# Optimization experiments

Hardware: AMD Instinct MI355X
Metric: run time of the kernel (lower is better)

The kernel has to match this reference:

```python
import jax, jax.numpy as jnp
import numpy as np

ROPE_BASE = 10000.0
CHUNK = 2048
NEG_INF = -1e30


def _rope(q, k, start_index):
    # q, k: (B, T, H, Dh) with Dh even; half-split RoPE as in RotaryEmbedding
    B, T, H, Dh = q.shape
    half = Dh // 2
    inv_freq = jnp.exp(jnp.arange(half, dtype=jnp.float32) * (-(np.log(ROPE_BASE) / half)))
    pos = jnp.arange(T, dtype=jnp.float32) + jnp.float32(start_index)
    ang = pos[:, None] * inv_freq[None, :]              # (T, half)
    cos = jnp.cos(ang)[None, :, None, :].astype(q.dtype)  # (1,T,1,half)
    sin = jnp.sin(ang)[None, :, None, :].astype(q.dtype)

    def rot(x):
        x1, x2 = x[..., :half], x[..., half:]
        return jnp.concatenate([x1 * cos - x2 * sin, x2 * cos + x1 * sin], axis=-1)

    return rot(q), rot(k)


def reference(q, k, v, start_index):
    # Chunked causal self-attention, softmax(QK^T) V with scale = 1.0 (Megalodon Eq. 9).
    B, T, H, Dh = q.shape
    Dv = v.shape[-1]
    q, k = _rope(q, k, start_index)

    nc = T // CHUNK  # T assumed multiple of chunk_size (prefill path, no cache)
    qc = q.reshape(B, nc, CHUNK, H, Dh)
    kc = k.reshape(B, nc, CHUNK, H, Dh)
    vc = v.reshape(B, nc, CHUNK, H, Dv)

    # per-chunk causal mask (C, C): 0 where j <= i else -inf
    i = jnp.arange(CHUNK)
    causal = (i[None, :] <= i[:, None])

    scores = jnp.einsum('bnqhd,bnkhd->bnhqk', qc, kc)  # scale = 1.0
    scores = jnp.where(causal[None, None, None, :, :], scores, NEG_INF)
    probs = jax.nn.softmax(scores, axis=-1)
    out = jnp.einsum('bnhqk,bnkhd->bnqhd', probs, vc)
    return out.reshape(B, T, H, Dv)


def setup_inputs() -> dict:
    key = jax.random.key(0)
    kq, kk, kv = jax.random.split(key, 3)
    B, T, H, Dh, Dv = 2, 4096, 16, 128, 128
    return {
        'q': jax.random.normal(kq, (B, T, H, Dh), dtype=jnp.float32),
        'k': jax.random.normal(kk, (B, T, H, Dh), dtype=jnp.float32),
        'v': jax.random.normal(kv, (B, T, H, Dv), dtype=jnp.float32),
        'start_index': 0,
    }
```

## Files before the change

### kernel.cpp

```cpp
#include <hip/hip_runtime.h>


#define T_TOT  4096
#define HH     16
#define DH     128
#define CHUNKL 2048
#define QT     128
#define KTILE  64
#define NEGV   1e30f
#define L2E    1.44269504088896f
#define THRL2  11.5415603f

typedef _Float16 f16;
typedef __attribute__((ext_vector_type(8)))  _Float16 f16x8;
typedef __attribute__((ext_vector_type(4)))  _Float16 f16x4;
typedef __attribute__((ext_vector_type(4)))  float    f32x4;

#define AS_G(p) ((const __attribute__((address_space(1))) void*)(p))
#define AS_L(p) ((__attribute__((address_space(3))) void*)(p))

__device__ __forceinline__ f32x4 mfma16(f16x8 a, f16x8 b, f32x4 c) {
    return __builtin_amdgcn_mfma_f32_16x16x32_f16(a, b, c, 0, 0, 0);
}

__global__ void rope_table_kernel(float* __restrict__ tab, const int* __restrict__ startp) {
    int gid = blockIdx.x * blockDim.x + threadIdx.x;
    int t = gid >> 6, d = gid & 63;
    float pos  = (float)(t + *startp);
    float invf = expf((float)d * (-9.210340371976184f / 64.0f));
    float s, c;
    sincosf(pos * invf, &s, &c);
    tab[gid] = c;
    tab[T_TOT * 64 + gid] = s;
}

__global__ void prep_kv_kernel(const float* __restrict__ K, const float* __restrict__ V,
                               const float* __restrict__ tab,
                               f16* __restrict__ Kws, f16* __restrict__ VTws) {
    const int half = (2 * T_TOT * HH * DH) / 8;
    int gid = blockIdx.x * blockDim.x + threadIdx.x;
    if (gid < half) {
        const int tile = gid >> 10, idx = gid & 1023;
        const int key = idx >> 4, c8 = idx & 15;
        const int dsw0 = c8 << 3;
        const int d0   = dsw0 ^ ((key & 15) << 3);
        const int kt = tile & 31, h = (tile >> 5) & 15, n = (tile >> 9) & 1, b = tile >> 10;
        const int t  = n * CHUNKL + kt * KTILE + key;
        const float* kp = K + ((size_t)(b * T_TOT + t) * HH + h) * DH;
        const int dl = d0 & 63;
        f32x4 xm0 = *(const f32x4*)(kp + d0);
        f32x4 xm1 = *(const f32x4*)(kp + d0 + 4);
        f32x4 xo0 = *(const f32x4*)(kp + (d0 ^ 64));
        f32x4 xo1 = *(const f32x4*)(kp + (d0 ^ 64) + 4);
        f32x4 cc0 = *(const f32x4*)(tab + t * 64 + dl);
        f32x4 cc1 = *(const f32x4*)(tab + t * 64 + dl + 4);
        f32x4 ss0 = *(const f32x4*)(tab + T_TOT * 64 + t * 64 + dl);
        f32x4 ss1 = *(const f32x4*)(tab + T_TOT * 64 + t * 64 + dl + 4);
        const float sgn = (d0 < 64) ? -1.f : 1.f;
        f16x8 out;
#pragma unroll
        for (int j = 0; j < 4; ++j) {
            out[j]     = (f16)(xm0[j] * cc0[j] + sgn * xo0[j] * ss0[j]);
            out[4 + j] = (f16)(xm1[j] * cc1[j] + sgn * xo1[j] * ss1[j]);
        }
        *(f16x8*)&Kws[(size_t)tile * 8192 + key * DH + dsw0] = out;
    } else {
        const int oc = gid - half;
        const int tile = oc >> 10, idx = oc & 1023;
        const int d = idx >> 3, c8 = idx & 7;
        const int ksw0 = c8 << 3;
        const int key0 = ksw0 ^ ((d & 7) << 3);
        const int kt = tile & 31, h = (tile >> 5) & 15, n = (tile >> 9) & 1, b = tile >> 10;
        const int t0 = n * CHUNKL + kt * KTILE + key0;
        const float* vp = V + ((size_t)(b * T_TOT + t0) * HH + h) * DH + d;
        f16x8 out;
#pragma unroll
        for (int j = 0; j < 8; ++j)
            out[j] = (f16)vp[(size_t)j * (HH * DH)];
        *(f16x8*)&VTws[(size_t)tile * 8192 + d * KTILE + ksw0] = out;
    }
}

__global__ __launch_bounds__(512, 4)
void attn_fast_kernel(const float* __restrict__ Q, const f16* __restrict__ Kws,
                      const f16* __restrict__ VTws, const float* __restrict__ tab,
                      float* __restrict__ O)
{
    __shared__ f16 Kl[2][KTILE * DH];
    __shared__ f16 VTl[2][KTILE * DH];
    __shared__ f16 Pl[8][16 * 64];

    const int bid = blockIdx.x;
    const int sb  = (bid & 7) * 128 + (bid >> 3);
    const int qt  = 15 - (sb & 15);
    const int bnh = sb >> 4;
    const int hd = bnh & 15, n = (bnh >> 4) & 1, b = bnh >> 5;

    const int tid = threadIdx.x;
    const int w   = tid >> 6;
    const int l   = tid & 63;
    const int g   = l >> 4;
    const int m   = l & 15;

    const int q0 = qt * QT;
    const size_t bh = (size_t)b * T_TOT * (HH * DH) + (size_t)hd * DH;
    const size_t tile0 = (size_t)bnh * (32 * 8192);

    const int qr = q0 + w * 16 + m;
    const int tg = n * CHUNKL + qr;
    const float* qp = Q + bh + (size_t)tg * (HH * DH);

    f16x8 qf[4];
#pragma unroll
    for (int kc = 0; kc < 4; ++kc) {
        const int dbase = kc * 32 + g * 8;
        const int dl    = dbase & 63;
        f32x4 xa0 = *(const f32x4*)(qp + dbase);
        f32x4 xa1 = *(const f32x4*)(qp + dbase + 4);
        f32x4 xb0 = *(const f32x4*)(qp + (dbase ^ 64));
        f32x4 xb1 = *(const f32x4*)(qp + (dbase ^ 64) + 4);
        float cc[8], ss[8];
        *(f32x4*)&cc[0] = *(const f32x4*)(tab + tg * 64 + dl);
        *(f32x4*)&cc[4] = *(const f32x4*)(tab + tg * 64 + dl + 4);
        *(f32x4*)&ss[0] = *(const f32x4*)(tab + T_TOT * 64 + tg * 64 + dl);
        *(f32x4*)&ss[4] = *(const f32x4*)(tab + T_TOT * 64 + tg * 64 + dl + 4);
        const float sgn = (dbase < 64) ? -1.f : 1.f;
        float xa[8] = {xa0[0],xa0[1],xa0[2],xa0[3],xa1[0],xa1[1],xa1[2],xa1[3]};
        float xb[8] = {xb0[0],xb0[1],xb0[2],xb0[3],xb1[0],xb1[1],xb1[2],xb1[3]};
        f16x8 f;
#pragma unroll
        for (int j = 0; j < 8; ++j)
            f[j] = (f16)((xa[j] * cc[j] + sgn * xb[j] * ss[j]) * L2E);
        qf[kc] = f;
    }

    f32x4 o[8];
    float mrun = -NEGV, lrun = 0.f;
    const f32x4 ZERO4 = {0.f, 0.f, 0.f, 0.f};
#pragma unroll
    for (int dt = 0; dt < 8; ++dt) o[dt] = ZERO4;

    const int nkt = 2 * qt + 2;

#define STAGE_TILE(t, bufi)                                                              \
    do {                                                                                 \
        const f16* ks_ = Kws  + tile0 + (size_t)(t) * 8192;                              \
        const f16* vs_ = VTws + tile0 + (size_t)(t) * 8192;                              \
        __builtin_amdgcn_global_load_lds(AS_G(ks_ + tid * 8),                            \
                                         AS_L(&Kl[bufi][tid * 8]), 16, 0, 0);            \
        __builtin_amdgcn_global_load_lds(AS_G(ks_ + 4096 + tid * 8),                     \
                                         AS_L(&Kl[bufi][4096 + tid * 8]), 16, 0, 0);     \
        __builtin_amdgcn_global_load_lds(AS_G(vs_ + tid * 8),                            \
                                         AS_L(&VTl[bufi][tid * 8]), 16, 0, 0);           \
        __builtin_amdgcn_global_load_lds(AS_G(vs_ + 4096 + tid * 8),                     \
                                         AS_L(&VTl[bufi][4096 + tid * 8]), 16, 0, 0);    \
    } while (0)

    STAGE_TILE(0, 0);
    STAGE_TILE(1, 1);

    for (int kt = 0; kt < nkt; ++kt) {
        if (kt + 1 < nkt) {
            asm volatile("s_waitcnt vmcnt(4)" ::: "memory");
        } else {
            asm volatile("s_waitcnt vmcnt(0)" ::: "memory");
        }
        __builtin_amdgcn_s_barrier();
        __builtin_amdgcn_sched_barrier(0);

        const int cur = kt & 1;
        const bool active = (kt * KTILE) < (q0 + w * 16 + 16);
        if (active) {
            const f16* Klc  = Kl[cur];
            const f16* VTlc = VTl[cur];

            f32x4 s[4];
#pragma unroll
            for (int ts = 0; ts < 4; ++ts) s[ts] = ZERO4;

            __builtin_amdgcn_s_setprio(1);
#pragma unroll
            for (int kc = 0; kc < 4; ++kc) {
#pragma unroll
                for (int ts = 0; ts < 4; ++ts) {
                    const int key = ts * 16 + m;
                    f16x8 kf = *(const f16x8*)&Klc[key * DH + ((kc * 32 + 8 * g) ^ (m * 8))];
                    s[ts] = mfma16(kf, qf[kc], s[ts]);
                }
            }
            __builtin_amdgcn_s_setprio(0);

            if ((kt + 1) * KTILE > q0 + w * 16) {
#pragma unroll
                for (int ts = 0; ts < 4; ++ts)
#pragma unroll
                    for (int r = 0; r < 4; ++r) {
                        const int key = kt * KTILE + ts * 16 + 4 * g + r;
                        if (key > qr) s[ts][r] = -NEGV;
                    }
            }

            float mx0 = fmaxf(fmaxf(s[0][0], s[0][1]), fmaxf(s[0][2], s[0][3]));
            float mx1 = fmaxf(fmaxf(s[1][0], s[1][1]), fmaxf(s[1][2], s[1][3]));
            float mx2 = fmaxf(fmaxf(s[2][0], s[2][1]), fmaxf(s[2][2], s[2][3]));
            float mx3 = fmaxf(fmaxf(s[3][0], s[3][1]), fmaxf(s[3][2], s[3][3]));
            float mx  = fmaxf(fmaxf(mx0, mx1), fmaxf(mx2, mx3));
            mx = fmaxf(mx, __shfl_xor(mx, 16));
            mx = fmaxf(mx, __shfl_xor(mx, 32));

            if (__any(mx > mrun + THRL2)) {
                const float mn = fmaxf(mrun, mx);
                const float al = exp2f(mrun - mn);
                mrun = mn;
                lrun *= al;
#pragma unroll
                for (int dt = 0; dt < 8; ++dt)
#pragma unroll
                    for (int r = 0; r < 4; ++r) o[dt][r] *= al;
            }

#pragma unroll
            for (int ts = 0; ts < 4; ++ts)
#pragma unroll
                for (int r = 0; r < 4; ++r) s[ts][r] = exp2f(s[ts][r] - mrun);
            {
                float p0 = (s[0][0] + s[0][1]) + (s[0][2] + s[0][3]);
                float p1 = (s[1][0] + s[1][1]) + (s[1][2] + s[1][3]);
                float p2 = (s[2][0] + s[2][1]) + (s[2][2] + s[2][3]);
                float p3 = (s[3][0] + s[3][1]) + (s[3][2] + s[3][3]);
                lrun += (p0 + p1) + (p2 + p3);
            }

#pragma unroll
            for (int ts = 0; ts < 4; ++ts) {
                f16x4 pk;
                pk[0] = (f16)s[ts][0];
                pk[1] = (f16)s[ts][1];
                pk[2] = (f16)s[ts][2];
                pk[3] = (f16)s[ts][3];
                const int blk = (2 * ts + (g >> 1)) ^ (m & 7);
                *(f16x4*)&Pl[w][m * 64 + blk * 8 + (g & 1) * 4] = pk;
            }

            __builtin_amdgcn_s_setprio(1);
#pragma unroll
            for (int kc = 0; kc < 2; ++kc) {
                f16x8 pb = *(const f16x8*)&Pl[w][m * 64 + ((kc * 4 + g) ^ (m & 7)) * 8];
#pragma unroll
                for (int dt = 0; dt < 8; ++dt) {
                    const int d = dt * 16 + m;
                    f16x8 vf = *(const f16x8*)&VTlc[d * KTILE + ((kc * 32 + 8 * g) ^ ((m & 7) * 8))];
                    o[dt] = mfma16(vf, pb, o[dt]);
                }
            }
            __builtin_amdgcn_s_setprio(0);
        }

        __builtin_amdgcn_s_barrier();
        if (kt + 2 < nkt) STAGE_TILE(kt + 2, cur);
    }
#undef STAGE_TILE

    float lt = lrun;
    lt += __shfl_xor(lt, 16);
    lt += __shfl_xor(lt, 32);
    const float inv = 1.0f / lt;
    float* op = O + bh + (size_t)tg * (HH * DH);
#pragma unroll
    for (int dt = 0; dt < 8; ++dt) {
        f32x4 val;
#pragma unroll
        for (int r = 0; r < 4; ++r) val[r] = o[dt][r] * inv;
        *(f32x4*)&op[dt * 16 + 4 * g] = val;
    }
}

__global__ __launch_bounds__(256, 2)
void attn_kernel(const float* __restrict__ Q, const float* __restrict__ K,
                 const float* __restrict__ V, const int* __restrict__ startp,
                 float* __restrict__ O)
{
    __shared__ f16 Kl[KTILE * DH];
    __shared__ f16 VTl[DH * KTILE];
    __shared__ f16 Pl[4][32 * 72];

    const int bid = blockIdx.x;
    const int qt  = 15 - (bid & 15);
    const int bnh = bid >> 4;
    const int h = bnh & 15, n = (bnh >> 4) & 1, b = bnh >> 5;

    const int tid  = threadIdx.x;
    const int w    = tid >> 6;
    const int lane = tid & 63;
    const int g    = lane >> 4, m = lane & 15;

    const int q0 = qt * QT;
    const size_t bh = (size_t)b * T_TOT * (HH * DH) + (size_t)h * DH;
    const int start = *startp;

    f16x8  qf[2][4];
    float  mrun[2][4], lrun[2][4];
    f32x4  o[2][8];
    const f32x4 ZERO4 = {0.f, 0.f, 0.f, 0.f};

#pragma unroll
    for (int rs = 0; rs < 2; ++rs) {
#pragma unroll
        for (int r = 0; r < 4; ++r) { mrun[rs][r] = -NEGV; lrun[rs][r] = 0.f; }
#pragma unroll
        for (int dt = 0; dt < 8; ++dt) o[rs][dt] = ZERO4;

        const int tg = n * CHUNKL + q0 + w * 32 + rs * 16 + m;
        const float* qp = Q + bh + (size_t)tg * (HH * DH);
#pragma unroll
        for (int kc = 0; kc < 4; ++kc) {
            const int dbase = kc * 32 + g * 8;
            const int dlo   = dbase & 63;
            f32x4 xa0 = *(const f32x4*)(qp + dbase);
            f32x4 xa1 = *(const f32x4*)(qp + dbase + 4);
            f32x4 xb0 = *(const f32x4*)(qp + (dbase ^ 64));
            f32x4 xb1 = *(const f32x4*)(qp + (dbase ^ 64) + 4);
            float cc[8], ss[8];
#pragma unroll
            for (int j = 0; j < 8; ++j) {
                float invf = expf((float)(dlo + j) * (-9.210340371976184f / 64.0f));
                sincosf((float)(tg + start) * invf, &ss[j], &cc[j]);
            }
            const float sgn = (dbase < 64) ? -1.f : 1.f;
            float xa[8] = {xa0[0],xa0[1],xa0[2],xa0[3],xa1[0],xa1[1],xa1[2],xa1[3]};
            float xb[8] = {xb0[0],xb0[1],xb0[2],xb0[3],xb1[0],xb1[1],xb1[2],xb1[3]};
            f16x8 f;
#pragma unroll
            for (int j = 0; j < 8; ++j) f[j] = (f16)(xa[j] * cc[j] + sgn * xb[j] * ss[j]);
            qf[rs][kc] = f;
        }
    }

    const int nkt = 2 * qt + 2;
    for (int kt = 0; kt < nkt; ++kt) {
        __syncthreads();
#pragma unroll
        for (int it = 0; it < 4; ++it) {
            const int tau = tid + 256 * it;
            const int row = tau >> 4;
            const int d0  = (tau & 15) << 2;
            const int tg  = n * CHUNKL + kt * KTILE + row;
            const float* kp = K + bh + (size_t)tg * (HH * DH);
            f32x4 xa = *(const f32x4*)(kp + d0);
            f32x4 xb = *(const f32x4*)(kp + d0 + 64);
            f32x4 cc, ss;
#pragma unroll
            for (int j = 0; j < 4; ++j) {
                float invf = expf((float)(d0 + j) * (-9.210340371976184f / 64.0f));
                float sv, cv;
                sincosf((float)(tg + start) * invf, &sv, &cv);
                cc[j] = cv; ss[j] = sv;
            }
            f16x4 oA, oB;
#pragma unroll
            for (int j = 0; j < 4; ++j) {
                oA[j] = (f16)(xa[j] * cc[j] - xb[j] * ss[j]);
                oB[j] = (f16)(xb[j] * cc[j] + xa[j] * ss[j]);
            }
            const int sw = (row & 7) << 3;
            *(f16x4*)&Kl[row * DH + (d0 ^ sw)]        = oA;
            *(f16x4*)&Kl[row * DH + ((d0 + 64) ^ sw)] = oB;
        }
#pragma unroll
        for (int it = 0; it < 8; ++it) {
            const int tau = tid + 256 * it;
            const int key = tau & 63;
            const int d0  = (tau >> 6) << 2;
            const int tg  = n * CHUNKL + kt * KTILE + key;
            f32x4 x = *(const f32x4*)(V + bh + (size_t)tg * (HH * DH) + d0);
#pragma unroll
            for (int j = 0; j < 4; ++j) {
                const int d = d0 + j;
                VTl[d * KTILE + (key ^ ((d & 7) << 3))] = (f16)x[j];
            }
        }
        __syncthreads();

        const bool active = (kt * KTILE) < (q0 + w * 32 + 32);
        if (active) {
            f32x4 sa[2][4];
#pragma unroll
            for (int rs = 0; rs < 2; ++rs)
#pragma unroll
                for (int nt = 0; nt < 4; ++nt) sa[rs][nt] = ZERO4;
#pragma unroll
            for (int nt = 0; nt < 4; ++nt) {
                const int key = nt * 16 + m;
                const int swk = (key & 7) << 3;
#pragma unroll
                for (int kc = 0; kc < 4; ++kc) {
                    f16x8 bf = *(const f16x8*)&Kl[key * DH + ((kc * 32 + g * 8) ^ swk)];
                    sa[0][nt] = mfma16(qf[0][kc], bf, sa[0][nt]);
                    sa[1][nt] = mfma16(qf[1][kc], bf, sa[1][nt]);
                }
            }
            const bool domask = (kt >= 2 * qt);
#pragma unroll
            for (int rs = 0; rs < 2; ++rs) {
                if (domask) {
#pragma unroll
                    for (int nt = 0; nt < 4; ++nt) {
                        const int key = kt * KTILE + nt * 16 + m;
#pragma unroll
                        for (int r = 0; r < 4; ++r) {
                            const int qr = q0 + w * 32 + rs * 16 + 4 * g + r;
                            if (key > qr) sa[rs][nt][r] = -NEGV;
                        }
                    }
                }
                float mx[4];
#pragma unroll
                for (int r = 0; r < 4; ++r)
                    mx[r] = fmaxf(fmaxf(sa[rs][0][r], sa[rs][1][r]),
                                  fmaxf(sa[rs][2][r], sa[rs][3][r]));
#pragma unroll
                for (int off = 1; off < 16; off <<= 1)
#pragma unroll
                    for (int r = 0; r < 4; ++r)
                        mx[r] = fmaxf(mx[r], __shfl_xor(mx[r], off));
                float al[4], ps[4];
#pragma unroll
                for (int r = 0; r < 4; ++r) {
                    const float mn = fmaxf(mrun[rs][r], mx[r]);
                    al[r] = exp2f((mrun[rs][r] - mn) * L2E);
                    mrun[rs][r] = mn;
                    ps[r] = 0.f;
                }
#pragma unroll
                for (int nt = 0; nt < 4; ++nt)
#pragma unroll
                    for (int r = 0; r < 4; ++r) {
                        const float p = exp2f((sa[rs][nt][r] - mrun[rs][r]) * L2E);
                        sa[rs][nt][r] = p;
                        ps[r] += p;
                    }
#pragma unroll
                for (int off = 1; off < 16; off <<= 1)
#pragma unroll
                    for (int r = 0; r < 4; ++r)
                        ps[r] += __shfl_xor(ps[r], off);
#pragma unroll
                for (int r = 0; r < 4; ++r)
                    lrun[rs][r] = lrun[rs][r] * al[r] + ps[r];
#pragma unroll
                for (int dt = 0; dt < 8; ++dt)
#pragma unroll
                    for (int r = 0; r < 4; ++r)
                        o[rs][dt][r] *= al[r];
#pragma unroll
                for (int nt = 0; nt < 4; ++nt)
#pragma unroll
                    for (int r = 0; r < 4; ++r)
                        Pl[w][(rs * 16 + 4 * g + r) * 72 + nt * 16 + m] = (f16)sa[rs][nt][r];
            }
            f16x8 pa[2][2];
#pragma unroll
            for (int rs = 0; rs < 2; ++rs)
#pragma unroll
                for (int kc = 0; kc < 2; ++kc)
                    pa[rs][kc] = *(const f16x8*)&Pl[w][(rs * 16 + m) * 72 + kc * 32 + g * 8];
#pragma unroll
            for (int dt = 0; dt < 8; ++dt) {
                const int d   = dt * 16 + m;
                const int swv = (d & 7) << 3;
#pragma unroll
                for (int kc = 0; kc < 2; ++kc) {
                    f16x8 vf = *(const f16x8*)&VTl[d * KTILE + ((kc * 32 + g * 8) ^ swv)];
                    o[0][dt] = mfma16(pa[0][kc], vf, o[0][dt]);
                    o[1][dt] = mfma16(pa[1][kc], vf, o[1][dt]);
                }
            }
        }
    }

#pragma unroll
    for (int rs = 0; rs < 2; ++rs) {
#pragma unroll
        for (int r = 0; r < 4; ++r) {
            const float inv = 1.0f / lrun[rs][r];
            const int tg = n * CHUNKL + q0 + w * 32 + rs * 16 + 4 * g + r;
            float* op = O + bh + (size_t)tg * (HH * DH);
#pragma unroll
            for (int dt = 0; dt < 8; ++dt)
                op[dt * 16 + m] = o[rs][dt][r] * inv;
        }
    }
}

extern "C" void kernel_launch(void* const* d_in, const int* in_sizes, int n_in,
                              void* d_out, int out_size, void* d_ws, size_t ws_size,
                              hipStream_t stream) {
    const float* q = (const float*)d_in[0];
    const float* k = (const float*)d_in[1];
    const float* v = (const float*)d_in[2];
    const int* start = (const int*)d_in[3];
    float* out = (float*)d_out;

    const size_t tab_elems = (size_t)2 * T_TOT * 64;
    const size_t kv_elems  = (size_t)2 * T_TOT * HH * DH;
    const size_t need = tab_elems * sizeof(float) + 2 * kv_elems * sizeof(f16);

    if (ws_size >= need) {
        float* tab = (float*)d_ws;
        f16* Kws  = (f16*)((char*)d_ws + tab_elems * sizeof(float));
        f16* VTws = Kws + kv_elems;
        rope_table_kernel<<<(T_TOT * 64) / 256, 256, 0, stream>>>(tab, start);
        prep_kv_kernel<<<(int)(2 * (kv_elems / 8) / 256), 256, 0, stream>>>(k, v, tab, Kws, VTws);
        attn_fast_kernel<<<1024, 512, 0, stream>>>(q, Kws, VTws, tab, out);
    } else {
        attn_kernel<<<64 * 16, 256, 0, stream>>>(q, k, v, start, out);
    }
}
```

Baseline: 210.3 us.

## Drop K/V double buffering and raise occupancy target in fast attention kernel

Replaces the two-stage prefetch pipeline for K and V^T tiles with a single LDS buffer. Each iteration now loads the tile, synchronizes, computes, then synchronizes again, which cuts LDS use per block so more blocks can reside on a CU. The launch bound's minimum-blocks hint rises from 4 to 6, which tightens the per-thread register budget. In exchange, global-to-LDS loads no longer overlap with MFMA work, and the tighter register cap may cause spills of the accumulator and Q fragments.

```diff
diff --git a/kernel.cpp b/kernel.cpp
--- a/kernel.cpp
+++ b/kernel.cpp
@@ -81,13 +81,13 @@
     }
 }
 
-__global__ __launch_bounds__(512, 4)
+__global__ __launch_bounds__(512, 6)
 void attn_fast_kernel(const float* __restrict__ Q, const f16* __restrict__ Kws,
                       const f16* __restrict__ VTws, const float* __restrict__ tab,
                       float* __restrict__ O)
 {
-    __shared__ f16 Kl[2][KTILE * DH];
-    __shared__ f16 VTl[2][KTILE * DH];
+    __shared__ f16 Kl[KTILE * DH];
+    __shared__ f16 VTl[KTILE * DH];
     __shared__ f16 Pl[8][16 * 64];
 
     const int bid = blockIdx.x;
@@ -142,38 +142,19 @@
 
     const int nkt = 2 * qt + 2;
 
-#define STAGE_TILE(t, bufi)                                                              \
-    do {                                                                                 \
-        const f16* ks_ = Kws  + tile0 + (size_t)(t) * 8192;                              \
-        const f16* vs_ = VTws + tile0 + (size_t)(t) * 8192;                              \
-        __builtin_amdgcn_global_load_lds(AS_G(ks_ + tid * 8),                            \
-                                         AS_L(&Kl[bufi][tid * 8]), 16, 0, 0);            \
-        __builtin_amdgcn_global_load_lds(AS_G(ks_ + 4096 + tid * 8),                     \
-                                         AS_L(&Kl[bufi][4096 + tid * 8]), 16, 0, 0);     \
-        __builtin_amdgcn_global_load_lds(AS_G(vs_ + tid * 8),                            \
-                                         AS_L(&VTl[bufi][tid * 8]), 16, 0, 0);           \
-        __builtin_amdgcn_global_load_lds(AS_G(vs_ + 4096 + tid * 8),                     \
-                                         AS_L(&VTl[bufi][4096 + tid * 8]), 16, 0, 0);    \
-    } while (0)
-
-    STAGE_TILE(0, 0);
-    STAGE_TILE(1, 1);
-
     for (int kt = 0; kt < nkt; ++kt) {
-        if (kt + 1 < nkt) {
-            asm volatile("s_waitcnt vmcnt(4)" ::: "memory");
-        } else {
-            asm volatile("s_waitcnt vmcnt(0)" ::: "memory");
-        }
-        __builtin_amdgcn_s_barrier();
-        __builtin_amdgcn_sched_barrier(0);
-
-        const int cur = kt & 1;
+        {
+            const f16* ks_ = Kws  + tile0 + (size_t)kt * 8192;
+            const f16* vs_ = VTws + tile0 + (size_t)kt * 8192;
+            __builtin_amdgcn_global_load_lds(AS_G(ks_ + tid * 8),        AS_L(&Kl[tid * 8]),         16, 0, 0);
+            __builtin_amdgcn_global_load_lds(AS_G(ks_ + 4096 + tid * 8), AS_L(&Kl[4096 + tid * 8]),  16, 0, 0);
+            __builtin_amdgcn_global_load_lds(AS_G(vs_ + tid * 8),        AS_L(&VTl[tid * 8]),        16, 0, 0);
+            __builtin_amdgcn_global_load_lds(AS_G(vs_ + 4096 + tid * 8), AS_L(&VTl[4096 + tid * 8]), 16, 0, 0);
+        }
+        __syncthreads();
+
         const bool active = (kt * KTILE) < (q0 + w * 16 + 16);
         if (active) {
-            const f16* Klc  = Kl[cur];
-            const f16* VTlc = VTl[cur];
-
             f32x4 s[4];
 #pragma unroll
             for (int ts = 0; ts < 4; ++ts) s[ts] = ZERO4;
@@ -184,7 +165,7 @@
 #pragma unroll
                 for (int ts = 0; ts < 4; ++ts) {
                     const int key = ts * 16 + m;
-                    f16x8 kf = *(const f16x8*)&Klc[key * DH + ((kc * 32 + 8 * g) ^ (m * 8))];
+                    f16x8 kf = *(const f16x8*)&Kl[key * DH + ((kc * 32 + 8 * g) ^ (m * 8))];
                     s[ts] = mfma16(kf, qf[kc], s[ts]);
                 }
             }
@@ -200,11 +181,11 @@
                     }
             }
 
-            float mx0 = fmaxf(fmaxf(s[0][0], s[0][1]), fmaxf(s[0][2], s[0][3]));
-            float mx1 = fmaxf(fmaxf(s[1][0], s[1][1]), fmaxf(s[1][2], s[1][3]));
-            float mx2 = fmaxf(fmaxf(s[2][0], s[2][1]), fmaxf(s[2][2], s[2][3]));
-            float mx3 = fmaxf(fmaxf(s[3][0], s[3][1]), fmaxf(s[3][2], s[3][3]));
-            float mx  = fmaxf(fmaxf(mx0, mx1), fmaxf(mx2, mx3));
+            float ma = fmaxf(fmaxf(s[0][0], s[0][1]), fmaxf(s[0][2], s[0][3]));
+            float mb = fmaxf(fmaxf(s[1][0], s[1][1]), fmaxf(s[1][2], s[1][3]));
+            float mc = fmaxf(fmaxf(s[2][0], s[2][1]), fmaxf(s[2][2], s[2][3]));
+            float md = fmaxf(fmaxf(s[3][0], s[3][1]), fmaxf(s[3][2], s[3][3]));
+            float mx = fmaxf(fmaxf(ma, mb), fmaxf(mc, md));
             mx = fmaxf(mx, __shfl_xor(mx, 16));
             mx = fmaxf(mx, __shfl_xor(mx, 32));
 
@@ -249,17 +230,15 @@
 #pragma unroll
                 for (int dt = 0; dt < 8; ++dt) {
                     const int d = dt * 16 + m;
-                    f16x8 vf = *(const f16x8*)&VTlc[d * KTILE + ((kc * 32 + 8 * g) ^ ((m & 7) * 8))];
+                    f16x8 vf = *(const f16x8*)&VTl[d * KTILE + ((kc * 32 + 8 * g) ^ ((m & 7) * 8))];
                     o[dt] = mfma16(vf, pb, o[dt]);
                 }
             }
             __builtin_amdgcn_s_setprio(0);
         }
 
-        __builtin_amdgcn_s_barrier();
-        if (kt + 2 < nkt) STAGE_TILE(kt + 2, cur);
-    }
-#undef STAGE_TILE
+        __syncthreads();
+    }
 
     float lt = lrun;
     lt += __shfl_xor(lt, 16);
```

Result: slower. 316.9 us (+50.7%).
